# Optimization experiments

Measured on AMD Instinct MI355X. Metric: run time of the kernel, lower is better.

Reference implementation:

```python
import jax, jax.numpy as jnp
import numpy as np
from jax import lax

PATCH = 32  # enc conv kernel/stride
EPS = 1e-12  # F.normalize eps


def setup_inputs() -> dict:
    key = jax.random.key(0)
    ks = jax.random.split(key, 7)
    B, N, H, W = 32, 256, 32, 32
    fdim, vdim = 512, 128
    x = jax.random.normal(ks[0], (B, 3 * N, H, W), dtype=jnp.float32)
    conv_w = jax.random.normal(ks[1], (fdim, 3, PATCH, PATCH), dtype=jnp.float32) * (1.0 / np.sqrt(3 * PATCH * PATCH))
    conv_b = jax.random.normal(ks[2], (fdim,), dtype=jnp.float32) * 0.01
    fc1_w = jax.random.normal(ks[3], (vdim, fdim), dtype=jnp.float32) * (1.0 / np.sqrt(fdim))
    fc1_b = jax.random.normal(ks[4], (vdim,), dtype=jnp.float32) * 0.01
    # deterministic dropout masks (p=0.5, train mode -> keep * 1/(1-p))
    drop1 = (jax.random.uniform(ks[5], (B, N, N)) >= 0.5).astype(jnp.float32) * 2.0
    drop2 = (jax.random.uniform(ks[6], (B, N, N)) >= 0.5).astype(jnp.float32) * 2.0
    return {"x": x, "conv_w": conv_w, "conv_b": conv_b,
            "fc1_w": fc1_w, "fc1_b": fc1_b, "drop1": drop1, "drop2": drop2}


def _branch(scores, drop, eye):
    # softmax over dim=-2, zero diag, dropout, L1-normalize over dim=-2
    P = jax.nn.softmax(scores, axis=-2)
    P = P * (1.0 - eye)
    P = P * drop
    denom = jnp.maximum(jnp.sum(jnp.abs(P), axis=-2, keepdims=True), EPS)
    return P / denom


def reference(x, conv_w, conv_b, fc1_w, fc1_b, drop1, drop2):
    B, C, H, W = x.shape
    N = C // 3
    xi = x.reshape(B * N, 3, H, W)
    # enc: patchify conv -> (B*N, fdim, 1, 1)
    fm = lax.conv_general_dilated(xi, conv_w, (PATCH, PATCH), 'VALID',
                                  dimension_numbers=('NCHW', 'OIHW', 'NCHW'))
    fm = fm + conv_b[None, :, None, None]
    # map2vec: adaptive avgpool(1,1) + flatten + fc1
    v = fm.mean(axis=(2, 3))                      # (B*N, fdim)
    v = v @ fc1_w.T + fc1_b                       # (B*N, vdim)
    f = v.reshape(B, N, -1)                       # (B, N, vdim)
    f_norm = f / jnp.maximum(jnp.linalg.norm(f, axis=-1, keepdims=True), EPS)
    A = jnp.einsum('bnd,bmd->bnm', f_norm, f_norm)  # cosine affinity (B,N,N)
    Atemp = A * (128.0 ** 0.5)                    # torch.div(A, 1/128**0.5)
    eye = jnp.eye(N, dtype=A.dtype)
    A1 = _branch(Atemp, drop1, eye)
    A2t = _branch(jnp.swapaxes(Atemp, -1, -2), drop2, eye)
    AtA = jnp.swapaxes(jnp.matmul(A2t, A1), -1, -2)
    # nll_loss(AtA, arange targets) == -mean of diagonal entries
    diag = jnp.einsum('bii->bi', AtA)
    loss = -jnp.mean(diag)
    return f, A, loss
```

## Files before the change

kernel.cpp:

```cpp
#include <hip/hip_runtime.h>

#define S_SCALE 11.313708498984761f
#define EPS 1e-12f

typedef __bf16 bf16x8 __attribute__((ext_vector_type(8)));
typedef float  f32x4  __attribute__((ext_vector_type(4)));

__device__ __forceinline__ f32x4 mfma16(bf16x8 a, bf16x8 b, f32x4 c) {
  return __builtin_amdgcn_mfma_f32_16x16x32_bf16(a, b, c, 0, 0, 0);
}

__device__ __forceinline__ float waveSum(float v) {
#pragma unroll
  for (int m = 32; m > 0; m >>= 1) v += __shfl_xor(v, m, 64);
  return v;
}

#define OFF_W    0
#define OFF_BIAS 786432
#define OFF_FN   786944
#define OFF_ZP   2884096
#define OFF_WTMP 2884096

__global__ __launch_bounds__(256) void k_bias(const float* __restrict__ fc1_w,
                                              const float* __restrict__ conv_b,
                                              const float* __restrict__ fc1_b,
                                              float* __restrict__ bias2,
                                              float* __restrict__ loss) {
  const int o = blockIdx.x, t = threadIdx.x;
  if (o == 0 && t == 0) loss[0] = 0.f;
  float p = fc1_w[o * 512 + t] * conv_b[t] +
            fc1_w[o * 512 + 256 + t] * conv_b[256 + t];
  p = waveSum(p);
  __shared__ float red[4];
  if ((t & 63) == 0) red[t >> 6] = p;
  __syncthreads();
  if (t == 0) bias2[o] = red[0] + red[1] + red[2] + red[3] + fc1_b[o];
}

__global__ __launch_bounds__(256) void k_fusew(const float* __restrict__ conv_w,
                                               const float* __restrict__ fc1_w,
                                               float* __restrict__ Wtmp) {
  __shared__ float cw_s[64][36];
  __shared__ float fc1_s[128][65];
  const int t = threadIdx.x;
  const int kt = blockIdx.x, cs = blockIdx.y;
  const int k0 = kt * 32;
  const int og = t >> 3, kg = t & 7;
  float acc[4][4] = {};
  for (int half = 0; half < 2; ++half) {
    const int cc = cs * 128 + half * 64;
    __syncthreads();
#pragma unroll
    for (int i = 0; i < 8; ++i) {
      int idx = t + 256 * i;
      int cr = idx >> 5, kk = idx & 31;
      cw_s[cr][kk] = conv_w[(cc + cr) * 3072 + k0 + kk];
    }
#pragma unroll
    for (int i = 0; i < 8; ++i) {
      int idx = t + 256 * i;
      int o = idx >> 4, c4 = (idx & 15) * 4;
      float4 v = *(const float4*)&fc1_w[o * 512 + cc + c4];
      fc1_s[o][c4 + 0] = v.x; fc1_s[o][c4 + 1] = v.y;
      fc1_s[o][c4 + 2] = v.z; fc1_s[o][c4 + 3] = v.w;
    }
    __syncthreads();
    for (int ci = 0; ci < 64; ++ci) {
      float4 cw = *(const float4*)&cw_s[ci][kg * 4];
#pragma unroll
      for (int j = 0; j < 4; ++j) {
        float fv = fc1_s[og * 4 + j][ci];
        acc[j][0] = fmaf(fv, cw.x, acc[j][0]);
        acc[j][1] = fmaf(fv, cw.y, acc[j][1]);
        acc[j][2] = fmaf(fv, cw.z, acc[j][2]);
        acc[j][3] = fmaf(fv, cw.w, acc[j][3]);
      }
    }
  }
  float* wp = Wtmp + cs * 393216;
#pragma unroll
  for (int j = 0; j < 4; ++j)
#pragma unroll
    for (int q = 0; q < 4; ++q)
      wp[(og * 4 + j) * 3072 + k0 + kg * 4 + q] = acc[j][q];
}

__global__ void k_cvtw(const float* __restrict__ Wtmp, __bf16* __restrict__ W) {
  int idx = blockIdx.x * 256 + threadIdx.x;
  float s = Wtmp[idx] + Wtmp[idx + 393216] + Wtmp[idx + 786432] +
            Wtmp[idx + 1179648];
  W[idx] = (__bf16)s;
}

#define PF(CC, AB, BB)                                               \
  {                                                                  \
    const float* an = ap + (CC) * 128;                               \
    const __bf16* bn0 = bp0 + (CC) * 128;                            \
    const __bf16* bn1 = bp1 + (CC) * 128;                            \
    _Pragma("unroll") for (int ks = 0; ks < 4; ++ks) {               \
      AB[ks][0] = *(const float4*)(an + ks * 32);                    \
      AB[ks][1] = *(const float4*)(an + ks * 32 + 4);                \
      BB[ks][0] = *(const uint4*)(bn0 + ks * 32);                    \
      BB[ks][1] = *(const uint4*)(bn1 + ks * 32);                    \
    }                                                                \
  }

#define COMP(AB, BB)                                                 \
  {                                                                  \
    _Pragma("unroll") for (int ks = 0; ks < 4; ++ks) {               \
      union { __bf16 h[8]; bf16x8 v; } pa;                           \
      float4 lo = AB[ks][0], hi = AB[ks][1];                         \
      pa.h[0] = (__bf16)lo.x; pa.h[1] = (__bf16)lo.y;                \
      pa.h[2] = (__bf16)lo.z; pa.h[3] = (__bf16)lo.w;                \
      pa.h[4] = (__bf16)hi.x; pa.h[5] = (__bf16)hi.y;                \
      pa.h[6] = (__bf16)hi.z; pa.h[7] = (__bf16)hi.w;                \
      acc0 = mfma16(pa.v, *(const bf16x8*)&BB[ks][0], acc0);         \
      acc1 = mfma16(pa.v, *(const bf16x8*)&BB[ks][1], acc1);         \
    }                                                                \
  }

__global__ __launch_bounds__(512) void k_gemm1(const float* __restrict__ x,
                                               const __bf16* __restrict__ W,
                                               const float* __restrict__ bias2,
                                               float* __restrict__ f,
                                               __bf16* __restrict__ fn) {
  const int t = threadIdx.x;
  const int wave = t >> 6, lane = t & 63;
  const int l15 = lane & 15, quad = lane >> 4;
  const int mhalf = wave & 1;
  const int nw = wave >> 1;
  const int m0 = blockIdx.x * 32;
  const int arow = m0 + mhalf * 16 + l15;
  const int n0 = nw * 32;
  const float* ap = x + arow * 3072 + quad * 8;
  const __bf16* bp0 = W + (n0 + l15) * 3072 + quad * 8;
  const __bf16* bp1 = bp0 + 16 * 3072;

  f32x4 acc0 = {0.f, 0.f, 0.f, 0.f}, acc1 = {0.f, 0.f, 0.f, 0.f};
  float4 ab0[4][2], ab1[4][2];
  uint4 bb0[4][2], bb1[4][2];
  PF(0, ab0, bb0)
  for (int c = 0; c < 24; c += 2) {
    if (c + 1 < 24) PF(c + 1, ab1, bb1)
    COMP(ab0, bb0)
    if (c + 2 < 24) PF(c + 2, ab0, bb0)
    COMP(ab1, bb1)
  }

  __shared__ float ssq[32];
  if (t < 32) ssq[t] = 0.f;
  __syncthreads();
  float bv0 = bias2[n0 + l15], bv1 = bias2[n0 + 16 + l15];
  float v0[4], v1[4];
#pragma unroll
  for (int r = 0; r < 4; ++r) {
    v0[r] = acc0[r] + bv0;
    v1[r] = acc1[r] + bv1;
    float part = v0[r] * v0[r] + v1[r] * v1[r];
#pragma unroll
    for (int m = 1; m < 16; m <<= 1) part += __shfl_xor(part, m, 64);
    if (l15 == 0) atomicAdd(&ssq[mhalf * 16 + quad * 4 + r], part);
  }
  __syncthreads();
#pragma unroll
  for (int r = 0; r < 4; ++r) {
    int lrow = mhalf * 16 + quad * 4 + r;
    int grow = m0 + lrow;
    float inv = 1.f / fmaxf(sqrtf(ssq[lrow]), EPS);
    f[grow * 128 + n0 + l15] = v0[r];
    f[grow * 128 + n0 + 16 + l15] = v1[r];
    fn[grow * 128 + n0 + l15] = (__bf16)(v0[r] * inv);
    fn[grow * 128 + n0 + 16 + l15] = (__bf16)(v1[r] * inv);
  }
}

__global__ __launch_bounds__(256) void k_gemm2(const __bf16* __restrict__ fn,
                                               float* __restrict__ Aout) {
  __shared__ __align__(16) __bf16 Li[64][136];
  __shared__ __align__(16) __bf16 Lj[64][136];
  const int t = threadIdx.x;
  const int b = blockIdx.y;
  const int ti = blockIdx.x >> 2, tj = blockIdx.x & 3;
  const int i0 = ti * 64, j0 = tj * 64;
  const int wave = t >> 6, lane = t & 63;
  const int l15 = lane & 15, quad = lane >> 4;
  const __bf16* fb = fn + b * 32768;
#pragma unroll
  for (int i = 0; i < 4; ++i) {
    int idx = t + 256 * i;
    int r = idx >> 4, c8 = (idx & 15) * 8;
    *(uint4*)&Li[r][c8] = *(const uint4*)&fb[(i0 + r) * 128 + c8];
    *(uint4*)&Lj[r][c8] = *(const uint4*)&fb[(j0 + r) * 128 + c8];
  }
  __syncthreads();
  f32x4 acc[4] = {{0.f, 0.f, 0.f, 0.f}, {0.f, 0.f, 0.f, 0.f},
                  {0.f, 0.f, 0.f, 0.f}, {0.f, 0.f, 0.f, 0.f}};
#pragma unroll
  for (int ks = 0; ks < 4; ++ks) {
    bf16x8 af = *(const bf16x8*)&Li[wave * 16 + l15][ks * 32 + quad * 8];
#pragma unroll
    for (int nt = 0; nt < 4; ++nt) {
      bf16x8 bf = *(const bf16x8*)&Lj[nt * 16 + l15][ks * 32 + quad * 8];
      acc[nt] = mfma16(af, bf, acc[nt]);
    }
  }
  float* Ab = Aout + b * 65536;
#pragma unroll
  for (int nt = 0; nt < 4; ++nt) {
    int gj = j0 + nt * 16 + l15;
#pragma unroll
    for (int r = 0; r < 4; ++r) {
      int gi = i0 + wave * 16 + quad * 4 + r;
      Ab[gi * 256 + gj] = acc[nt][r];
    }
  }
}

__global__ __launch_bounds__(256) void k_z(const float* __restrict__ Aout,
                                           const float* __restrict__ d1,
                                           const float* __restrict__ d2,
                                           float* __restrict__ Zp) {
  const int t = threadIdx.x;
  const int b = blockIdx.y, nc = blockIdx.x;
  const int base = b * 65536;
  float z1 = 0.f, z2 = 0.f;
  for (int r = 0; r < 32; ++r) {
    int n = nc * 32 + r;
    int idx = base + n * 256 + t;
    float a = Aout[idx];
    float e = __expf(fmaf(S_SCALE, a, -S_SCALE));
    if (n != t) {
      z1 = fmaf(e, d1[idx], z1);
      z2 = fmaf(e, d2[idx], z2);
    }
  }
  Zp[nc * 8192 + b * 256 + t] = z1;
  Zp[(8 + nc) * 8192 + b * 256 + t] = z2;
}

__global__ __launch_bounds__(256) void k_loss(const float* __restrict__ Aout,
                                              const float* __restrict__ d1,
                                              const float* __restrict__ d2,
                                              const float* __restrict__ Zp,
                                              float* __restrict__ loss) {
  __shared__ float d1s[64][65];
  __shared__ float z1s[64], z2s[64];
  __shared__ float red[4];
  const int t = threadIdx.x;
  const int b = blockIdx.y;
  const int ic = blockIdx.x >> 2, kc = blockIdx.x & 3;
  const int i0 = ic * 64, k0 = kc * 64;
  const int base = b * 65536;
  if (t < 64) {
    float s = 0.f;
#pragma unroll
    for (int p = 0; p < 8; ++p) s += Zp[p * 8192 + b * 256 + i0 + t];
    z1s[t] = 1.f / fmaxf(s, EPS);
  } else if (t < 128) {
    float s = 0.f;
#pragma unroll
    for (int p = 0; p < 8; ++p) s += Zp[(8 + p) * 8192 + b * 256 + k0 + t - 64];
    z2s[t - 64] = 1.f / fmaxf(s, EPS);
  }
#pragma unroll
  for (int ii = 0; ii < 16; ++ii) {
    int idx = t + 256 * ii;
    int kr = idx >> 6, ci = idx & 63;
    d1s[kr][ci] = d1[base + (k0 + kr) * 256 + i0 + ci];
  }
  __syncthreads();
  const int kl = t & 63, ig = t >> 6;
  float inv2 = z2s[kl];
  float accv = 0.f;
  for (int ii = 0; ii < 16; ++ii) {
    int il = ig * 16 + ii;
    int idx = base + (i0 + il) * 256 + k0 + kl;
    float a = Aout[idx];
    float e = __expf(fmaf(2.f * S_SCALE, a, -2.f * S_SCALE));
    float v = e * d2[idx] * d1s[kl][il] * z1s[il] * inv2;
    if (i0 + il != k0 + kl) accv += v;
  }
  accv = waveSum(accv);
  if ((t & 63) == 0) red[t >> 6] = accv;
  __syncthreads();
  if (t == 0) {
    float tot = red[0] + red[1] + red[2] + red[3];
    atomicAdd(loss, tot * (-1.f / 8192.f));
  }
}

extern "C" void kernel_launch(void* const* d_in, const int* in_sizes, int n_in,
                              void* d_out, int out_size, void* d_ws,
                              size_t ws_size, hipStream_t stream) {
  const float* x = (const float*)d_in[0];
  const float* conv_w = (const float*)d_in[1];
  const float* conv_b = (const float*)d_in[2];
  const float* fc1_w = (const float*)d_in[3];
  const float* fc1_b = (const float*)d_in[4];
  const float* drop1 = (const float*)d_in[5];
  const float* drop2 = (const float*)d_in[6];
  char* ws = (char*)d_ws;
  __bf16* W = (__bf16*)(ws + OFF_W);
  float* bias2 = (float*)(ws + OFF_BIAS);
  __bf16* fn = (__bf16*)(ws + OFF_FN);
  float* Zp = (float*)(ws + OFF_ZP);
  float* Wtmp = (float*)(ws + OFF_WTMP);
  float* f = (float*)d_out;
  float* Aout = f + 1048576;
  float* loss = f + 3145728;

  k_bias<<<128, 256, 0, stream>>>(fc1_w, conv_b, fc1_b, bias2, loss);
  k_fusew<<<dim3(96, 4), 256, 0, stream>>>(conv_w, fc1_w, Wtmp);
  k_cvtw<<<1536, 256, 0, stream>>>(Wtmp, W);
  k_gemm1<<<256, 512, 0, stream>>>(x, W, bias2, f, fn);
  k_gemm2<<<dim3(16, 32), 256, 0, stream>>>(fn, Aout);
  k_z<<<dim3(8, 32), 256, 0, stream>>>(Aout, drop1, drop2, Zp);
  k_loss<<<dim3(16, 32), 256, 0, stream>>>(Aout, drop1, drop2, Zp, loss);
}
```

Measured before the change: 285.8 us.

## Restructure pipeline: fuse weight convert, split-K gemm1 with LDS loads, fold Z into gemm2

The fused-weight kernel now loops over all input channels and writes bf16 directly, which removes the separate conversion kernel and the fp32 partial buffer. The first GEMM is split into two K halves over a 2D grid, with the activation tile staged through swizzled LDS using direct global-to-LDS loads. A new finalize kernel adds the two partials and the bias, then normalizes each row. The softmax column-sum (Z) computation moves into the affinity GEMM epilogue so the standalone Z pass no longer rereads A. This trades an extra partial-sum write and read plus one more launch for better gemm1 parallelism and fewer kernels overall.

```diff
diff --git a/kernel.cpp b/kernel.cpp
--- a/kernel.cpp
+++ b/kernel.cpp
@@ -1,4 +1,5 @@
 #include <hip/hip_runtime.h>
+#include <stdint.h>
 
 #define S_SCALE 11.313708498984761f
 #define EPS 1e-12f
@@ -14,13 +15,19 @@
 #pragma unroll
   for (int m = 32; m > 0; m >>= 1) v += __shfl_xor(v, m, 64);
   return v;
+}
+
+__device__ __forceinline__ void load_lds16(const float* g, float* l) {
+  __builtin_amdgcn_global_load_lds(
+      (const __attribute__((address_space(1))) uint32_t*)g,
+      (__attribute__((address_space(3))) uint32_t*)l, 16, 0, 0);
 }
 
 #define OFF_W    0
 #define OFF_BIAS 786432
 #define OFF_FN   786944
 #define OFF_ZP   2884096
-#define OFF_WTMP 2884096
+#define OFF_P1   3146240
 
 __global__ __launch_bounds__(256) void k_bias(const float* __restrict__ fc1_w,
                                               const float* __restrict__ conv_b,
@@ -38,18 +45,18 @@
   if (t == 0) bias2[o] = red[0] + red[1] + red[2] + red[3] + fc1_b[o];
 }
 
-__global__ __launch_bounds__(256) void k_fusew(const float* __restrict__ conv_w,
-                                               const float* __restrict__ fc1_w,
-                                               float* __restrict__ Wtmp) {
+__global__ __launch_bounds__(256) void k_fusew2(const float* __restrict__ conv_w,
+                                                const float* __restrict__ fc1_w,
+                                                __bf16* __restrict__ W) {
   __shared__ float cw_s[64][36];
   __shared__ float fc1_s[128][65];
   const int t = threadIdx.x;
-  const int kt = blockIdx.x, cs = blockIdx.y;
+  const int kt = blockIdx.x;
   const int k0 = kt * 32;
   const int og = t >> 3, kg = t & 7;
   float acc[4][4] = {};
-  for (int half = 0; half < 2; ++half) {
-    const int cc = cs * 128 + half * 64;
+  for (int cs = 0; cs < 8; ++cs) {
+    const int cc = cs * 64;
     __syncthreads();
 #pragma unroll
     for (int i = 0; i < 8; ++i) {
@@ -78,107 +85,113 @@
       }
     }
   }
-  float* wp = Wtmp + cs * 393216;
 #pragma unroll
   for (int j = 0; j < 4; ++j)
 #pragma unroll
     for (int q = 0; q < 4; ++q)
-      wp[(og * 4 + j) * 3072 + k0 + kg * 4 + q] = acc[j][q];
-}
-
-__global__ void k_cvtw(const float* __restrict__ Wtmp, __bf16* __restrict__ W) {
-  int idx = blockIdx.x * 256 + threadIdx.x;
-  float s = Wtmp[idx] + Wtmp[idx + 393216] + Wtmp[idx + 786432] +
-            Wtmp[idx + 1179648];
-  W[idx] = (__bf16)s;
-}
-
-#define PF(CC, AB, BB)                                               \
-  {                                                                  \
-    const float* an = ap + (CC) * 128;                               \
-    const __bf16* bn0 = bp0 + (CC) * 128;                            \
-    const __bf16* bn1 = bp1 + (CC) * 128;                            \
-    _Pragma("unroll") for (int ks = 0; ks < 4; ++ks) {               \
-      AB[ks][0] = *(const float4*)(an + ks * 32);                    \
-      AB[ks][1] = *(const float4*)(an + ks * 32 + 4);                \
-      BB[ks][0] = *(const uint4*)(bn0 + ks * 32);                    \
-      BB[ks][1] = *(const uint4*)(bn1 + ks * 32);                    \
-    }                                                                \
-  }
-
-#define COMP(AB, BB)                                                 \
-  {                                                                  \
-    _Pragma("unroll") for (int ks = 0; ks < 4; ++ks) {               \
-      union { __bf16 h[8]; bf16x8 v; } pa;                           \
-      float4 lo = AB[ks][0], hi = AB[ks][1];                         \
-      pa.h[0] = (__bf16)lo.x; pa.h[1] = (__bf16)lo.y;                \
-      pa.h[2] = (__bf16)lo.z; pa.h[3] = (__bf16)lo.w;                \
-      pa.h[4] = (__bf16)hi.x; pa.h[5] = (__bf16)hi.y;                \
-      pa.h[6] = (__bf16)hi.z; pa.h[7] = (__bf16)hi.w;                \
-      acc0 = mfma16(pa.v, *(const bf16x8*)&BB[ks][0], acc0);         \
-      acc1 = mfma16(pa.v, *(const bf16x8*)&BB[ks][1], acc1);         \
-    }                                                                \
-  }
-
-__global__ __launch_bounds__(512) void k_gemm1(const float* __restrict__ x,
+      W[(og * 4 + j) * 3072 + k0 + kg * 4 + q] = (__bf16)acc[j][q];
+}
+
+__global__ __launch_bounds__(256) void k_gemm1(const float* __restrict__ x,
                                                const __bf16* __restrict__ W,
-                                               const float* __restrict__ bias2,
-                                               float* __restrict__ f,
-                                               __bf16* __restrict__ fn) {
+                                               float* __restrict__ P0,
+                                               float* __restrict__ P1) {
+  __shared__ __align__(16) float A_lds[32 * 64];
   const int t = threadIdx.x;
   const int wave = t >> 6, lane = t & 63;
   const int l15 = lane & 15, quad = lane >> 4;
-  const int mhalf = wave & 1;
-  const int nw = wave >> 1;
   const int m0 = blockIdx.x * 32;
-  const int arow = m0 + mhalf * 16 + l15;
-  const int n0 = nw * 32;
-  const float* ap = x + arow * 3072 + quad * 8;
-  const __bf16* bp0 = W + (n0 + l15) * 3072 + quad * 8;
-  const __bf16* bp1 = bp0 + 16 * 3072;
-
-  f32x4 acc0 = {0.f, 0.f, 0.f, 0.f}, acc1 = {0.f, 0.f, 0.f, 0.f};
-  float4 ab0[4][2], ab1[4][2];
-  uint4 bb0[4][2], bb1[4][2];
-  PF(0, ab0, bb0)
-  for (int c = 0; c < 24; c += 2) {
-    if (c + 1 < 24) PF(c + 1, ab1, bb1)
-    COMP(ab0, bb0)
-    if (c + 2 < 24) PF(c + 2, ab0, bb0)
-    COMP(ab1, bb1)
-  }
-
-  __shared__ float ssq[32];
-  if (t < 32) ssq[t] = 0.f;
-  __syncthreads();
-  float bv0 = bias2[n0 + l15], bv1 = bias2[n0 + 16 + l15];
-  float v0[4], v1[4];
-#pragma unroll
-  for (int r = 0; r < 4; ++r) {
-    v0[r] = acc0[r] + bv0;
-    v1[r] = acc1[r] + bv1;
-    float part = v0[r] * v0[r] + v1[r] * v1[r];
-#pragma unroll
-    for (int m = 1; m < 16; m <<= 1) part += __shfl_xor(part, m, 64);
-    if (l15 == 0) atomicAdd(&ssq[mhalf * 16 + quad * 4 + r], part);
-  }
-  __syncthreads();
-#pragma unroll
-  for (int r = 0; r < 4; ++r) {
-    int lrow = mhalf * 16 + quad * 4 + r;
-    int grow = m0 + lrow;
-    float inv = 1.f / fmaxf(sqrtf(ssq[lrow]), EPS);
-    f[grow * 128 + n0 + l15] = v0[r];
-    f[grow * 128 + n0 + 16 + l15] = v1[r];
-    fn[grow * 128 + n0 + l15] = (__bf16)(v0[r] * inv);
-    fn[grow * 128 + n0 + 16 + l15] = (__bf16)(v1[r] * inv);
-  }
+  const int kbase = blockIdx.y * 1536;
+  float* P = blockIdx.y ? P1 : P0;
+
+  int dr[2], dc[2];
+#pragma unroll
+  for (int j = 0; j < 2; ++j) {
+    int row = wave * 8 + j * 4 + (lane >> 4);
+    int cl = (lane & 15) ^ (row & 15);
+    dr[j] = row;
+    dc[j] = cl * 4;
+  }
+
+  f32x4 acc[2][2] = {{{0.f,0.f,0.f,0.f},{0.f,0.f,0.f,0.f}},
+                     {{0.f,0.f,0.f,0.f},{0.f,0.f,0.f,0.f}}};
+  const __bf16* bp = W + (wave * 32 + l15) * 3072 + quad * 8;
+
+  for (int it = 0; it < 24; ++it) {
+    const int k0 = kbase + it * 64;
+    __syncthreads();
+#pragma unroll
+    for (int j = 0; j < 2; ++j)
+      load_lds16(x + (m0 + dr[j]) * 3072 + k0 + dc[j],
+                 &A_lds[(wave * 2 + j) * 256]);
+    uint4 breg[2][2];
+#pragma unroll
+    for (int ks = 0; ks < 2; ++ks)
+#pragma unroll
+      for (int ni = 0; ni < 2; ++ni)
+        breg[ks][ni] = *(const uint4*)(bp + ni * 16 * 3072 + k0 + ks * 32);
+    __syncthreads();
+#pragma unroll
+    for (int ks = 0; ks < 2; ++ks) {
+      bf16x8 afrag[2];
+#pragma unroll
+      for (int mi = 0; mi < 2; ++mi) {
+        const int rb = (l15 + mi * 16) * 64;
+        float4 lo = *(const float4*)&A_lds[rb + (((ks * 8 + quad * 2 + 0) ^ l15) << 2)];
+        float4 hi = *(const float4*)&A_lds[rb + (((ks * 8 + quad * 2 + 1) ^ l15) << 2)];
+        union { __bf16 h[8]; bf16x8 v; } pk;
+        pk.h[0] = (__bf16)lo.x; pk.h[1] = (__bf16)lo.y;
+        pk.h[2] = (__bf16)lo.z; pk.h[3] = (__bf16)lo.w;
+        pk.h[4] = (__bf16)hi.x; pk.h[5] = (__bf16)hi.y;
+        pk.h[6] = (__bf16)hi.z; pk.h[7] = (__bf16)hi.w;
+        afrag[mi] = pk.v;
+      }
+#pragma unroll
+      for (int mi = 0; mi < 2; ++mi)
+#pragma unroll
+        for (int ni = 0; ni < 2; ++ni)
+          acc[mi][ni] = mfma16(afrag[mi], *(const bf16x8*)&breg[ks][ni],
+                               acc[mi][ni]);
+    }
+  }
+#pragma unroll
+  for (int mi = 0; mi < 2; ++mi)
+#pragma unroll
+    for (int ni = 0; ni < 2; ++ni) {
+      int col = wave * 32 + ni * 16 + l15;
+#pragma unroll
+      for (int r = 0; r < 4; ++r) {
+        int row = m0 + mi * 16 + quad * 4 + r;
+        P[row * 128 + col] = acc[mi][ni][r];
+      }
+    }
+}
+
+__global__ __launch_bounds__(256) void k_fin(float* __restrict__ f_inout,
+                                             const float* __restrict__ P1,
+                                             const float* __restrict__ bias2,
+                                             __bf16* __restrict__ fn) {
+  const int wave = threadIdx.x >> 6, lane = threadIdx.x & 63;
+  const int row = blockIdx.x * 4 + wave;
+  const int i0 = row * 128 + lane, i1 = i0 + 64;
+  float v0 = f_inout[i0] + P1[i0] + bias2[lane];
+  float v1 = f_inout[i1] + P1[i1] + bias2[lane + 64];
+  float ss = waveSum(fmaf(v0, v0, v1 * v1));
+  float inv = 1.f / fmaxf(sqrtf(ss), EPS);
+  f_inout[i0] = v0;
+  f_inout[i1] = v1;
+  fn[i0] = (__bf16)(v0 * inv);
+  fn[i1] = (__bf16)(v1 * inv);
 }
 
 __global__ __launch_bounds__(256) void k_gemm2(const __bf16* __restrict__ fn,
-                                               float* __restrict__ Aout) {
+                                               const float* __restrict__ d1,
+                                               const float* __restrict__ d2,
+                                               float* __restrict__ Aout,
+                                               float* __restrict__ Zp) {
   __shared__ __align__(16) __bf16 Li[64][136];
   __shared__ __align__(16) __bf16 Lj[64][136];
+  __shared__ float zred[2][4][64];
   const int t = threadIdx.x;
   const int b = blockIdx.y;
   const int ti = blockIdx.x >> 2, tj = blockIdx.x & 3;
@@ -205,38 +218,45 @@
       acc[nt] = mfma16(af, bf, acc[nt]);
     }
   }
-  float* Ab = Aout + b * 65536;
+  const int base = b * 65536;
+  float* Ab = Aout + base;
+  float z1c[4] = {0.f, 0.f, 0.f, 0.f}, z2c[4] = {0.f, 0.f, 0.f, 0.f};
 #pragma unroll
   for (int nt = 0; nt < 4; ++nt) {
     int gj = j0 + nt * 16 + l15;
 #pragma unroll
     for (int r = 0; r < 4; ++r) {
       int gi = i0 + wave * 16 + quad * 4 + r;
-      Ab[gi * 256 + gj] = acc[nt][r];
-    }
-  }
-}
-
-__global__ __launch_bounds__(256) void k_z(const float* __restrict__ Aout,
-                                           const float* __restrict__ d1,
-                                           const float* __restrict__ d2,
-                                           float* __restrict__ Zp) {
-  const int t = threadIdx.x;
-  const int b = blockIdx.y, nc = blockIdx.x;
-  const int base = b * 65536;
-  float z1 = 0.f, z2 = 0.f;
-  for (int r = 0; r < 32; ++r) {
-    int n = nc * 32 + r;
-    int idx = base + n * 256 + t;
-    float a = Aout[idx];
-    float e = __expf(fmaf(S_SCALE, a, -S_SCALE));
-    if (n != t) {
-      z1 = fmaf(e, d1[idx], z1);
-      z2 = fmaf(e, d2[idx], z2);
-    }
-  }
-  Zp[nc * 8192 + b * 256 + t] = z1;
-  Zp[(8 + nc) * 8192 + b * 256 + t] = z2;
+      float a = acc[nt][r];
+      Ab[gi * 256 + gj] = a;
+      float e = __expf(fmaf(S_SCALE, a, -S_SCALE));
+      if (gi != gj) {
+        int idx = base + gi * 256 + gj;
+        z1c[nt] = fmaf(e, d1[idx], z1c[nt]);
+        z2c[nt] = fmaf(e, d2[idx], z2c[nt]);
+      }
+    }
+  }
+#pragma unroll
+  for (int nt = 0; nt < 4; ++nt) {
+    z1c[nt] += __shfl_xor(z1c[nt], 16, 64);
+    z1c[nt] += __shfl_xor(z1c[nt], 32, 64);
+    z2c[nt] += __shfl_xor(z2c[nt], 16, 64);
+    z2c[nt] += __shfl_xor(z2c[nt], 32, 64);
+  }
+  if (quad == 0) {
+#pragma unroll
+    for (int nt = 0; nt < 4; ++nt) {
+      zred[0][wave][nt * 16 + l15] = z1c[nt];
+      zred[1][wave][nt * 16 + l15] = z2c[nt];
+    }
+  }
+  __syncthreads();
+  if (t < 128) {
+    int z = t >> 6, c = t & 63;
+    float s = zred[z][0][c] + zred[z][1][c] + zred[z][2][c] + zred[z][3][c];
+    Zp[(z * 4 + ti) * 8192 + b * 256 + j0 + c] = s;
+  }
 }
 
 __global__ __launch_bounds__(256) void k_loss(const float* __restrict__ Aout,
@@ -255,12 +275,12 @@
   if (t < 64) {
     float s = 0.f;
 #pragma unroll
-    for (int p = 0; p < 8; ++p) s += Zp[p * 8192 + b * 256 + i0 + t];
+    for (int p = 0; p < 4; ++p) s += Zp[p * 8192 + b * 256 + i0 + t];
     z1s[t] = 1.f / fmaxf(s, EPS);
   } else if (t < 128) {
     float s = 0.f;
 #pragma unroll
-    for (int p = 0; p < 8; ++p) s += Zp[(8 + p) * 8192 + b * 256 + k0 + t - 64];
+    for (int p = 0; p < 4; ++p) s += Zp[(4 + p) * 8192 + b * 256 + k0 + t - 64];
     z2s[t - 64] = 1.f / fmaxf(s, EPS);
   }
 #pragma unroll
@@ -305,16 +325,15 @@
   float* bias2 = (float*)(ws + OFF_BIAS);
   __bf16* fn = (__bf16*)(ws + OFF_FN);
   float* Zp = (float*)(ws + OFF_ZP);
-  float* Wtmp = (float*)(ws + OFF_WTMP);
+  float* P1 = (float*)(ws + OFF_P1);
   float* f = (float*)d_out;
   float* Aout = f + 1048576;
   float* loss = f + 3145728;
 
   k_bias<<<128, 256, 0, stream>>>(fc1_w, conv_b, fc1_b, bias2, loss);
-  k_fusew<<<dim3(96, 4), 256, 0, stream>>>(conv_w, fc1_w, Wtmp);
-  k_cvtw<<<1536, 256, 0, stream>>>(Wtmp, W);
-  k_gemm1<<<256, 512, 0, stream>>>(x, W, bias2, f, fn);
-  k_gemm2<<<dim3(16, 32), 256, 0, stream>>>(fn, Aout);
-  k_z<<<dim3(8, 32), 256, 0, stream>>>(Aout, drop1, drop2, Zp);
+  k_fusew2<<<96, 256, 0, stream>>>(conv_w, fc1_w, W);
+  k_gemm1<<<dim3(256, 2), 256, 0, stream>>>(x, W, f, P1);
+  k_fin<<<2048, 256, 0, stream>>>(f, P1, bias2, fn);
+  k_gemm2<<<dim3(16, 32), 256, 0, stream>>>(fn, drop1, drop2, Aout, Zp);
   k_loss<<<dim3(16, 32), 256, 0, stream>>>(Aout, drop1, drop2, Zp, loss);
 }
```

After: 238.5 us. 16.5% less time.
